# Kernel tuning notes

Hardware: AMD Instinct MI355X
Metric: run time of the kernel (lower is better)

The kernel has to match this reference:

```python
import jax, jax.numpy as jnp
import numpy as np

H, DN, DR, DV, L = 16, 128, 64, 128, 512
EPS = 1e-6

def rotate_half(x):
    x1, x2 = jnp.split(x, 2, axis=-1)
    return jnp.concatenate((-x2, x1), axis=-1)

def setup_inputs() -> dict:
    key = jax.random.key(0)
    ks = jax.random.split(key, 8)
    B, S, HID = 2, 2048, 2048
    inv_freq = 1.0 / (10000.0 ** (jnp.arange(0, DR, 2, dtype=jnp.float32) / DR))
    pos = jnp.arange(B * S, dtype=jnp.float32)
    freqs = pos[:, None] * inv_freq[None, :]
    emb = jnp.concatenate((freqs, freqs), axis=-1)
    return {
        "hidden_states": jax.random.normal(ks[0], (B, S, HID), jnp.float32),
        "cos": jnp.cos(emb),
        "sin": jnp.sin(emb),
        "q_proj_w": jax.random.normal(ks[1], (H * (DN + DR), HID), jnp.float32) * 0.02,
        "kv_a_proj_w": jax.random.normal(ks[2], (L + DR, HID), jnp.float32) * 0.02,
        "kv_a_ln_w": jnp.ones((L,), jnp.float32),
        "W_UK_T": jax.random.normal(ks[3], (H, DN, L), jnp.float32) * 0.02,
        "W_UV": jax.random.normal(ks[4], (H, L, DV), jnp.float32) * 0.02,
        "o_proj_w": jax.random.normal(ks[5], (HID, H * DV), jnp.float32) * 0.02,
    }

def reference(hidden_states, cos, sin, q_proj_w, kv_a_proj_w, kv_a_ln_w, W_UK_T, W_UV, o_proj_w):
    B, S, HID = hidden_states.shape
    T = B * S
    x = hidden_states.reshape(T, HID)
    # q projection -> [T, H, DN+DR]
    q = (x @ q_proj_w.T).reshape(T, H, DN + DR)
    q_pass, q_rot = q[..., :DN], q[..., DN:]
    # compressed kv -> latent + rope key (MQA-style, shared across heads)
    ckv = x @ kv_a_proj_w.T  # [T, L+DR]
    k_pass, k_rot = ckv[..., :L], ckv[..., L:]
    kv_c = k_pass * jax.lax.rsqrt(jnp.mean(k_pass * k_pass, axis=-1, keepdims=True) + EPS) * kv_a_ln_w
    # interleaved RoPE (rope_interleave=True): de-interleave then rotate_half form
    q_rot = q_rot.reshape(T, H, DR // 2, 2).swapaxes(-1, -2).reshape(T, H, DR)
    k_rot = k_rot.reshape(T, DR // 2, 2).swapaxes(-1, -2).reshape(T, DR)
    q_rot = q_rot * cos[:, None, :] + rotate_half(q_rot) * sin[:, None, :]
    k_rot = k_rot * cos + rotate_half(k_rot) * sin
    # absorb W_UK into queries: [T,H,L]
    q_lat = jnp.einsum('thd,hdl->thl', q_pass, W_UK_T)
    q_lat = q_lat.reshape(B, S, H, L)
    q_rot = q_rot.reshape(B, S, H, DR)
    kv_c_b = kv_c.reshape(B, S, L)
    k_rot_b = k_rot.reshape(B, S, DR)
    scale = 1.0 / np.sqrt(DN + DR)
    scores = (jnp.einsum('bshl,btl->bhst', q_lat, kv_c_b)
              + jnp.einsum('bshd,btd->bhst', q_rot, k_rot_b)) * scale
    causal = jnp.tril(jnp.ones((S, S), dtype=bool))
    scores = jnp.where(causal[None, None], scores, jnp.float32(-1e30))
    attn = jax.nn.softmax(scores, axis=-1)
    out_lat = jnp.einsum('bhst,btl->bshl', attn, kv_c_b)   # [B,S,H,L]
    out = jnp.einsum('bshl,hlv->bshv', out_lat, W_UV)       # [B,S,H,DV]
    out = out.reshape(B, S, H * DV) @ o_proj_w.T
    return out
```

## Files before the change

### kernel.cpp

```cpp
#include <hip/hip_runtime.h>
#include <stdint.h>

#define T_TOK 4096
#define HIDD  2048
#define NH    16
#define DNN   128
#define DRR   64
#define DVV   128
#define LAT   512
#define DQK   576
#define SEQ   2048
#define NB    2
#define KSTR  592
#define KCH   2368

typedef __attribute__((__ext_vector_type__(8))) short short8;
typedef __attribute__((__ext_vector_type__(4))) float f32x4;

__device__ __forceinline__ float bf2f(ushort u) {
  union { uint32_t i; float f; } v; v.i = ((uint32_t)u) << 16; return v.f;
}
__device__ __forceinline__ ushort f2bf(float f) {
  union { float f; uint32_t i; } v; v.f = f;
  uint32_t r = v.i + 0x7FFF + ((v.i >> 16) & 1);
  return (ushort)(r >> 16);
}

__device__ __forceinline__ void gld_lds16(const void* g, void* l) {
  __builtin_amdgcn_global_load_lds((const __attribute__((address_space(1))) void*)g,
                                   (__attribute__((address_space(3))) void*)l, 16, 0, 0);
}

__global__ void cast4(const float* __restrict__ in, ushort* __restrict__ out, int n4) {
  int i = blockIdx.x * blockDim.x + threadIdx.x;
  if (i >= n4) return;
  float4 v = ((const float4*)in)[i];
  ushort4 o; o.x = f2bf(v.x); o.y = f2bf(v.y); o.z = f2bf(v.z); o.w = f2bf(v.w);
  ((ushort4*)out)[i] = o;
}

__global__ void cast_pad_kv(const float* __restrict__ in, ushort* __restrict__ out) {
  int i = blockIdx.x * 256 + threadIdx.x;
  int row = (i * 4) >> 11;
  ushort4 o;
  if (row < 576) {
    float4 v = ((const float4*)in)[i];
    o.x = f2bf(v.x); o.y = f2bf(v.y); o.z = f2bf(v.z); o.w = f2bf(v.w);
  } else { o.x = 0; o.y = 0; o.z = 0; o.w = 0; }
  ((ushort4*)out)[i] = o;
}

__global__ void cast_wuk(const float* __restrict__ in, ushort* __restrict__ out) {
  int o = blockIdx.x * 256 + threadIdx.x;
  int d = o & 127, l = (o >> 7) & 511, h = o >> 16;
  out[o] = f2bf(in[((size_t)(h * 128 + d)) * 512 + l]);
}
__global__ void cast_wuv(const float* __restrict__ in, ushort* __restrict__ out) {
  int o = blockIdx.x * 256 + threadIdx.x;
  int l = o & 511, v = (o >> 9) & 127, h = o >> 16;
  out[o] = f2bf(in[((size_t)(h * 512 + l)) * 128 + v]);
}

template<int OUT_BF16>
__global__ __launch_bounds__(256) void gemm_bt(
    const ushort* __restrict__ A, const ushort* __restrict__ B, void* __restrict__ Cv,
    int K, int lda, int ldb, int ldc,
    long long aB, long long bB, long long cB)
{
  __shared__ ushort As[128 * 32];
  __shared__ ushort Bs[128 * 32];
  const int tid = threadIdx.x;
  const int lane = tid & 63, wid = tid >> 6;
  const int m0 = blockIdx.y * 128, n0 = blockIdx.x * 128;
  A += (size_t)blockIdx.z * aB;
  B += (size_t)blockIdx.z * bB;
  const int wm = (wid >> 1) * 64, wn = (wid & 1) * 64;
  const int fr = lane & 15;
  const int kk = (lane >> 4) * 8;
  f32x4 acc[4][4] = {};
  for (int k0 = 0; k0 < K; k0 += 32) {
    __syncthreads();
#pragma unroll
    for (int i = 0; i < 2; ++i) {
      int c = i * 256 + tid;
      gld_lds16(A + (size_t)(m0 + (c >> 2)) * lda + k0 + (c & 3) * 8, (void*)(As + c * 8));
    }
#pragma unroll
    for (int i = 0; i < 2; ++i) {
      int c = i * 256 + tid;
      gld_lds16(B + (size_t)(n0 + (c >> 2)) * ldb + k0 + (c & 3) * 8, (void*)(Bs + c * 8));
    }
    __syncthreads();
    short8 af[4], bf[4];
#pragma unroll
    for (int x = 0; x < 4; ++x) af[x] = *(const short8*)(As + (wm + x * 16 + fr) * 32 + kk);
#pragma unroll
    for (int x = 0; x < 4; ++x) bf[x] = *(const short8*)(Bs + (wn + x * 16 + fr) * 32 + kk);
#pragma unroll
    for (int mi = 0; mi < 4; ++mi)
#pragma unroll
      for (int ni = 0; ni < 4; ++ni)
        acc[mi][ni] = __builtin_amdgcn_mfma_f32_16x16x32_bf16(af[mi], bf[ni], acc[mi][ni], 0, 0, 0);
  }
  const int rb = (lane >> 4) * 4;
#pragma unroll
  for (int mi = 0; mi < 4; ++mi)
#pragma unroll
    for (int ni = 0; ni < 4; ++ni)
#pragma unroll
      for (int r = 0; r < 4; ++r) {
        size_t row = (size_t)(m0 + wm + mi * 16 + rb + r);
        size_t col = (size_t)(n0 + wn + ni * 16 + fr);
        size_t idx = row * (size_t)ldc + col + (size_t)blockIdx.z * cB;
        if (OUT_BF16) ((ushort*)Cv)[idx] = f2bf(acc[mi][ni][r]);
        else          ((float*)Cv)[idx]  = acc[mi][ni][r];
      }
}

__global__ __launch_bounds__(256) void rms_rope_k(
    const float* __restrict__ ckvf, const float* __restrict__ lnw,
    const float* __restrict__ cosb, const float* __restrict__ sinb,
    ushort* __restrict__ k_eff)
{
  const int t = blockIdx.x, tid = threadIdx.x;
  __shared__ float red[4];
  float v0 = ckvf[(size_t)t * 640 + tid];
  float v1 = ckvf[(size_t)t * 640 + 256 + tid];
  float ss = v0 * v0 + v1 * v1;
#pragma unroll
  for (int m = 1; m < 64; m <<= 1) ss += __shfl_xor(ss, m);
  if ((tid & 63) == 0) red[tid >> 6] = ss;
  __syncthreads();
  float rn = rsqrtf((red[0] + red[1] + red[2] + red[3]) * (1.0f / 512.0f) + 1e-6f);
  k_eff[(size_t)t * KSTR + tid]       = f2bf(v0 * rn * lnw[tid]);
  k_eff[(size_t)t * KSTR + 256 + tid] = f2bf(v1 * rn * lnw[256 + tid]);
  if (tid < 64) {
    int j = tid;
    int src  = (j < 32) ? 2 * j : 2 * (j - 32) + 1;
    int psrc = (j < 32) ? src + 1 : src - 1;
    float xv = ckvf[(size_t)t * 640 + 512 + src];
    float pv = ckvf[(size_t)t * 640 + 512 + psrc];
    float c = cosb[t * 64 + j], s = sinb[t * 64 + j];
    k_eff[(size_t)t * KSTR + 512 + j] = f2bf((j < 32) ? xv * c - pv * s : xv * c + pv * s);
  }
}

__global__ __launch_bounds__(256) void transpose_kv(
    const ushort* __restrict__ keff, ushort* __restrict__ kvT)
{
  __shared__ ushort Tl[64][72];
  const int s0 = blockIdx.x * 64, v0 = blockIdx.y * 64, b = blockIdx.z;
  const int tid = threadIdx.x;
#pragma unroll
  for (int i = 0; i < 2; ++i) {
    int c = i * 256 + tid;
    int r = c >> 3, c8 = (c & 7) * 8;
    *(short8*)&Tl[r][c8] = *(const short8*)&keff[((size_t)b * SEQ + s0 + r) * KSTR + v0 + c8];
  }
  __syncthreads();
#pragma unroll
  for (int i = 0; i < 2; ++i) {
    int c = i * 256 + tid;
    int v = c >> 3, s8 = (c & 7) * 8;
    short8 o;
#pragma unroll
    for (int e = 0; e < 8; ++e) o[e] = Tl[s8 + e][v];
    *(short8*)&kvT[((size_t)b * 512 + v0 + v) * SEQ + s0 + s8] = o;
  }
}

__global__ void rope_q(const ushort* __restrict__ qb, const float* __restrict__ cosb,
                       const float* __restrict__ sinb, ushort* __restrict__ q_eff)
{
  const int t = blockIdx.x;
  const int h = blockIdx.y * 4 + threadIdx.y;
  const int j = threadIdx.x;
  size_t base = (size_t)t * 3072 + h * 192 + 128;
  int src  = (j < 32) ? 2 * j : 2 * (j - 32) + 1;
  int psrc = (j < 32) ? src + 1 : src - 1;
  float xv = bf2f(qb[base + src]), pv = bf2f(qb[base + psrc]);
  float c = cosb[t * 64 + j], s = sinb[t * 64 + j];
  q_eff[((size_t)h * T_TOK + t) * DQK + 512 + j] = f2bf((j < 32) ? xv * c - pv * s : xv * c + pv * s);
}

__global__ __launch_bounds__(512, 2) void attn3(
    const ushort* __restrict__ q_eff, const ushort* __restrict__ keff,
    const ushort* __restrict__ kvT, ushort* __restrict__ out_lat)
{
  const int pair = blockIdx.x;
  const int h = blockIdx.y, b = blockIdx.z;
  const int tid = threadIdx.x, lane = tid & 63, w = tid >> 6;
  __shared__ ushort Ks[2][32 * KSTR];
  __shared__ ushort Vt[2][512 * 32];
  __shared__ ushort Pl[8][16 * 40];

  const int fr = lane & 15, g = lane >> 4;

  auto stageK = [&](int kt, int buf) {
    const ushort* ksrc = keff + ((size_t)b * SEQ + (size_t)kt * 32) * KSTR;
    ushort* kd = &Ks[buf][0];
#pragma unroll
    for (int i = 0; i < 5; ++i) {
      int c0 = w * 320 + i * 64;
      if (c0 < KCH) {
        int c = c0 + lane;
        gld_lds16(ksrc + (size_t)c * 8, (void*)(kd + (size_t)c * 8));
      }
    }
  };
  auto stageV = [&](int kt, int buf) {
    const ushort* vsrc = kvT + (size_t)b * 512 * SEQ + (size_t)kt * 32;
    ushort* vd = &Vt[buf][0];
#pragma unroll
    for (int i = 0; i < 4; ++i) {
      int c = w * 256 + i * 64 + lane;
      gld_lds16(vsrc + (size_t)(c >> 2) * SEQ + (c & 3) * 8, (void*)(vd + (size_t)c * 8));
    }
  };

  for (int half = 0; half < 2; ++half) {
    const int qb = half ? pair : (15 - pair);
    const int q0 = qb * 128 + w * 16;

    const ushort* qrow = q_eff + ((size_t)h * T_TOK + (size_t)b * SEQ + q0 + fr) * DQK + g * 8;
    short8 qf[18];
#pragma unroll
    for (int ks = 0; ks < 18; ++ks) qf[ks] = *(const short8*)(qrow + ks * 32);

    f32x4 acc[32] = {};
    float m_s[4] = {-1e30f, -1e30f, -1e30f, -1e30f};
    float l_s[4] = {0.f, 0.f, 0.f, 0.f};

    const int nt = 4 * qb + 4;

    stageK(0, 0);
    stageV(0, 0);

    for (int kt = 0; kt < nt; ++kt) {
      const int cur = kt & 1;
      if (kt + 1 < nt) {
        stageK(kt + 1, cur ^ 1);
        stageV(kt + 1, cur ^ 1);
        if (w == 7) asm volatile("s_waitcnt vmcnt(6)" ::: "memory");
        else        asm volatile("s_waitcnt vmcnt(9)" ::: "memory");
      } else {
        asm volatile("s_waitcnt vmcnt(0)" ::: "memory");
      }
      __builtin_amdgcn_sched_barrier(0);
      __builtin_amdgcn_s_barrier();
      __builtin_amdgcn_sched_barrier(0);

      if (kt * 32 <= q0 + 15) {
        const ushort* Kc = &Ks[cur][0];
        const ushort* Vc = &Vt[cur][0];
        f32x4 s0 = {}, s1 = {};
#pragma unroll
        for (int ks = 0; ks < 18; ++ks) {
          short8 b0 = *(const short8*)(Kc + (0 * 16 + fr) * KSTR + ks * 32 + g * 8);
          short8 b1 = *(const short8*)(Kc + (1 * 16 + fr) * KSTR + ks * 32 + g * 8);
          s0 = __builtin_amdgcn_mfma_f32_16x16x32_bf16(qf[ks], b0, s0, 0, 0, 0);
          s1 = __builtin_amdgcn_mfma_f32_16x16x32_bf16(qf[ks], b1, s1, 0, 0, 0);
        }
        const float SC = 0.07216878364870322f;
        const bool diag = (kt * 32 + 31 > q0);
        float sv0[4], sv1[4];
#pragma unroll
        for (int r = 0; r < 4; ++r) {
          int qg = q0 + 4 * g + r;
          float a0 = s0[r] * SC, a1 = s1[r] * SC;
          if (diag) {
            if (kt * 32 + fr > qg)      a0 = -1e30f;
            if (kt * 32 + 16 + fr > qg) a1 = -1e30f;
          }
          sv0[r] = a0; sv1[r] = a1;
        }
        float mx[4];
#pragma unroll
        for (int r = 0; r < 4; ++r) {
          float m2 = fmaxf(sv0[r], sv1[r]);
          m2 = fmaxf(m2, __shfl_xor(m2, 1));
          m2 = fmaxf(m2, __shfl_xor(m2, 2));
          m2 = fmaxf(m2, __shfl_xor(m2, 4));
          m2 = fmaxf(m2, __shfl_xor(m2, 8));
          mx[r] = m2;
        }
        float need = mx[0] - m_s[0];
#pragma unroll
        for (int r = 1; r < 4; ++r) need = fmaxf(need, mx[r] - m_s[r]);
        if (__any(need > 8.0f)) {
          float rsc[4];
#pragma unroll
          for (int r = 0; r < 4; ++r) {
            float mn = fmaxf(m_s[r], mx[r]);
            rsc[r] = __expf(m_s[r] - mn);
            m_s[r] = mn;
            l_s[r] *= rsc[r];
          }
#pragma unroll
          for (int n2 = 0; n2 < 32; ++n2)
#pragma unroll
            for (int r = 0; r < 4; ++r) acc[n2][r] *= rsc[r];
        }
        float p0[4], p1[4];
#pragma unroll
        for (int r = 0; r < 4; ++r) {
          p0[r] = __expf(sv0[r] - m_s[r]);
          p1[r] = __expf(sv1[r] - m_s[r]);
          float ps = p0[r] + p1[r];
          ps += __shfl_xor(ps, 1);
          ps += __shfl_xor(ps, 2);
          ps += __shfl_xor(ps, 4);
          ps += __shfl_xor(ps, 8);
          l_s[r] += ps;
          Pl[w][(4 * g + r) * 40 + fr]      = f2bf(p0[r]);
          Pl[w][(4 * g + r) * 40 + 16 + fr] = f2bf(p1[r]);
        }
        short8 pa = *(const short8*)(Pl[w] + fr * 40 + g * 8);
#pragma unroll
        for (int n2 = 0; n2 < 32; ++n2) {
          short8 bv = *(const short8*)(Vc + (n2 * 16 + fr) * 32 + g * 8);
          acc[n2] = __builtin_amdgcn_mfma_f32_16x16x32_bf16(pa, bv, acc[n2], 0, 0, 0);
        }
      }
      __builtin_amdgcn_sched_barrier(0);
      __builtin_amdgcn_s_barrier();
      __builtin_amdgcn_sched_barrier(0);
    }

    const size_t obase = ((size_t)h * T_TOK + (size_t)b * SEQ + q0) * LAT;
    float inv[4];
#pragma unroll
    for (int r = 0; r < 4; ++r) inv[r] = 1.0f / l_s[r];
#pragma unroll
    for (int n2 = 0; n2 < 32; ++n2)
#pragma unroll
      for (int r = 0; r < 4; ++r)
        out_lat[obase + (size_t)(4 * g + r) * LAT + n2 * 16 + fr] = f2bf(acc[n2][r] * inv[r]);
  }
}

extern "C" void kernel_launch(void* const* d_in, const int* in_sizes, int n_in,
                              void* d_out, int out_size, void* d_ws, size_t ws_size,
                              hipStream_t stream) {
  const float* hs   = (const float*)d_in[0];
  const float* cosb = (const float*)d_in[1];
  const float* sinb = (const float*)d_in[2];
  const float* qw   = (const float*)d_in[3];
  const float* kvw  = (const float*)d_in[4];
  const float* lnw  = (const float*)d_in[5];
  const float* wuk  = (const float*)d_in[6];
  const float* wuv  = (const float*)d_in[7];
  const float* wo   = (const float*)d_in[8];
  float* out = (float*)d_out;
  char* ws = (char*)d_ws;

  const size_t o_xb   = 0;
  const size_t o_qb   = 16777216;
  const size_t o_wq   = 41943040;
  const size_t o_wkv  = 54525952;
  const size_t o_ckv  = 57147392;
  const size_t o_ol   = 0;
  const size_t o_wukt = 67633152;
  const size_t o_wuvt = 69730304;
  const size_t o_wo   = 71827456;
  const size_t o_keff = 80216064;
  const size_t o_qeff = 85065728;
  const size_t o_oh   = 160563200;
  const size_t o_kvt  = 177340416;

  ushort* xb    = (ushort*)(ws + o_xb);
  ushort* qbuf  = (ushort*)(ws + o_qb);
  ushort* wq_b  = (ushort*)(ws + o_wq);
  ushort* wkv_b = (ushort*)(ws + o_wkv);
  float*  ckvf  = (float*)(ws + o_ckv);
  ushort* olat  = (ushort*)(ws + o_ol);
  ushort* wukt  = (ushort*)(ws + o_wukt);
  ushort* wuvt  = (ushort*)(ws + o_wuvt);
  ushort* wo_b  = (ushort*)(ws + o_wo);
  ushort* keff  = (ushort*)(ws + o_keff);
  ushort* qeff  = (ushort*)(ws + o_qeff);
  ushort* ohead = (ushort*)(ws + o_oh);
  ushort* kvt   = (ushort*)(ws + o_kvt);

  cast4<<<8192, 256, 0, stream>>>(hs, xb, 8388608 / 4);
  cast4<<<6144, 256, 0, stream>>>(qw, wq_b, 6291456 / 4);
  cast_pad_kv<<<1280, 256, 0, stream>>>(kvw, wkv_b);
  cast4<<<4096, 256, 0, stream>>>(wo, wo_b, 4194304 / 4);
  cast_wuk<<<4096, 256, 0, stream>>>(wuk, wukt);
  cast_wuv<<<4096, 256, 0, stream>>>(wuv, wuvt);

  gemm_bt<1><<<dim3(24, 32, 1), 256, 0, stream>>>(xb, wq_b, qbuf, 2048, 2048, 2048, 3072, 0, 0, 0);
  gemm_bt<0><<<dim3(5, 32, 1), 256, 0, stream>>>(xb, wkv_b, ckvf, 2048, 2048, 2048, 640, 0, 0, 0);
  rms_rope_k<<<4096, 256, 0, stream>>>(ckvf, lnw, cosb, sinb, keff);
  transpose_kv<<<dim3(32, 8, 2), 256, 0, stream>>>(keff, kvt);
  rope_q<<<dim3(4096, 4, 1), dim3(64, 4, 1), 0, stream>>>(qbuf, cosb, sinb, qeff);
  gemm_bt<1><<<dim3(4, 32, 16), 256, 0, stream>>>(qbuf, wukt, qeff, 128, 3072, 128, 576,
                                                  192LL, 65536LL, 2359296LL);
  attn3<<<dim3(8, 16, 2), 512, 0, stream>>>(qeff, keff, kvt, olat);
  gemm_bt<1><<<dim3(1, 32, 16), 256, 0, stream>>>(olat, wuvt, ohead, 512, 512, 512, 2048,
                                                  2097152LL, 65536LL, 128LL);
  gemm_bt<0><<<dim3(16, 32, 1), 256, 0, stream>>>(ohead, wo_b, out, 2048, 2048, 2048, 2048, 0, 0, 0);
}
```

Baseline: 684.8 us.

## Double-buffer GEMM LDS staging and merge q and kv_a projections

The bf16 GEMM now double-buffers its LDS tiles and prefetches the next K slice while MFMAs run on the current one, using explicit vmcnt waits and barriers. The q projection and kv_a projection are merged into one GEMM with a 3712-wide output. The compressed-KV part now comes out as bf16 rather than fp32, and the downstream RMSNorm/RoPE and q-absorb kernels read from the merged buffer. This removes one launch and one pass over the activations and hides load latency, but the KV latent is now rounded to bf16 before normalization and the GEMM uses twice the LDS.

```diff
diff --git a/kernel.cpp b/kernel.cpp
--- a/kernel.cpp
+++ b/kernel.cpp
@@ -13,6 +13,7 @@
 #define NB    2
 #define KSTR  592
 #define KCH   2368
+#define QCKV  3712
 
 typedef __attribute__((__ext_vector_type__(8))) short short8;
 typedef __attribute__((__ext_vector_type__(4))) float f32x4;
@@ -67,8 +68,8 @@
     int K, int lda, int ldb, int ldc,
     long long aB, long long bB, long long cB)
 {
-  __shared__ ushort As[128 * 32];
-  __shared__ ushort Bs[128 * 32];
+  __shared__ ushort As[2][128 * 32];
+  __shared__ ushort Bs[2][128 * 32];
   const int tid = threadIdx.x;
   const int lane = tid & 63, wid = tid >> 6;
   const int m0 = blockIdx.y * 128, n0 = blockIdx.x * 128;
@@ -77,31 +78,51 @@
   const int wm = (wid >> 1) * 64, wn = (wid & 1) * 64;
   const int fr = lane & 15;
   const int kk = (lane >> 4) * 8;
-  f32x4 acc[4][4] = {};
-  for (int k0 = 0; k0 < K; k0 += 32) {
-    __syncthreads();
+
+  auto stage = [&](int k0, int buf) {
 #pragma unroll
     for (int i = 0; i < 2; ++i) {
       int c = i * 256 + tid;
-      gld_lds16(A + (size_t)(m0 + (c >> 2)) * lda + k0 + (c & 3) * 8, (void*)(As + c * 8));
+      gld_lds16(A + (size_t)(m0 + (c >> 2)) * lda + k0 + (c & 3) * 8, (void*)(&As[buf][0] + c * 8));
     }
 #pragma unroll
     for (int i = 0; i < 2; ++i) {
       int c = i * 256 + tid;
-      gld_lds16(B + (size_t)(n0 + (c >> 2)) * ldb + k0 + (c & 3) * 8, (void*)(Bs + c * 8));
-    }
-    __syncthreads();
+      gld_lds16(B + (size_t)(n0 + (c >> 2)) * ldb + k0 + (c & 3) * 8, (void*)(&Bs[buf][0] + c * 8));
+    }
+  };
+
+  f32x4 acc[4][4] = {};
+  const int nt = K >> 5;
+  stage(0, 0);
+  for (int t = 0; t < nt; ++t) {
+    const int cur = t & 1;
+    if (t + 1 < nt) {
+      stage((t + 1) << 5, cur ^ 1);
+      asm volatile("s_waitcnt vmcnt(4)" ::: "memory");
+    } else {
+      asm volatile("s_waitcnt vmcnt(0)" ::: "memory");
+    }
+    __builtin_amdgcn_sched_barrier(0);
+    __builtin_amdgcn_s_barrier();
+    __builtin_amdgcn_sched_barrier(0);
+
     short8 af[4], bf[4];
 #pragma unroll
-    for (int x = 0; x < 4; ++x) af[x] = *(const short8*)(As + (wm + x * 16 + fr) * 32 + kk);
-#pragma unroll
-    for (int x = 0; x < 4; ++x) bf[x] = *(const short8*)(Bs + (wn + x * 16 + fr) * 32 + kk);
+    for (int x = 0; x < 4; ++x) af[x] = *(const short8*)(&As[cur][0] + (wm + x * 16 + fr) * 32 + kk);
+#pragma unroll
+    for (int x = 0; x < 4; ++x) bf[x] = *(const short8*)(&Bs[cur][0] + (wn + x * 16 + fr) * 32 + kk);
 #pragma unroll
     for (int mi = 0; mi < 4; ++mi)
 #pragma unroll
       for (int ni = 0; ni < 4; ++ni)
         acc[mi][ni] = __builtin_amdgcn_mfma_f32_16x16x32_bf16(af[mi], bf[ni], acc[mi][ni], 0, 0, 0);
+
+    __builtin_amdgcn_sched_barrier(0);
+    __builtin_amdgcn_s_barrier();
+    __builtin_amdgcn_sched_barrier(0);
   }
+
   const int rb = (lane >> 4) * 4;
 #pragma unroll
   for (int mi = 0; mi < 4; ++mi)
@@ -118,14 +139,15 @@
 }
 
 __global__ __launch_bounds__(256) void rms_rope_k(
-    const float* __restrict__ ckvf, const float* __restrict__ lnw,
+    const ushort* __restrict__ qckv, const float* __restrict__ lnw,
     const float* __restrict__ cosb, const float* __restrict__ sinb,
     ushort* __restrict__ k_eff)
 {
   const int t = blockIdx.x, tid = threadIdx.x;
   __shared__ float red[4];
-  float v0 = ckvf[(size_t)t * 640 + tid];
-  float v1 = ckvf[(size_t)t * 640 + 256 + tid];
+  const size_t base = (size_t)t * QCKV + 3072;
+  float v0 = bf2f(qckv[base + tid]);
+  float v1 = bf2f(qckv[base + 256 + tid]);
   float ss = v0 * v0 + v1 * v1;
 #pragma unroll
   for (int m = 1; m < 64; m <<= 1) ss += __shfl_xor(ss, m);
@@ -138,8 +160,8 @@
     int j = tid;
     int src  = (j < 32) ? 2 * j : 2 * (j - 32) + 1;
     int psrc = (j < 32) ? src + 1 : src - 1;
-    float xv = ckvf[(size_t)t * 640 + 512 + src];
-    float pv = ckvf[(size_t)t * 640 + 512 + psrc];
+    float xv = bf2f(qckv[base + 512 + src]);
+    float pv = bf2f(qckv[base + 512 + psrc]);
     float c = cosb[t * 64 + j], s = sinb[t * 64 + j];
     k_eff[(size_t)t * KSTR + 512 + j] = f2bf((j < 32) ? xv * c - pv * s : xv * c + pv * s);
   }
@@ -175,7 +197,7 @@
   const int t = blockIdx.x;
   const int h = blockIdx.y * 4 + threadIdx.y;
   const int j = threadIdx.x;
-  size_t base = (size_t)t * 3072 + h * 192 + 128;
+  size_t base = (size_t)t * QCKV + h * 192 + 128;
   int src  = (j < 32) ? 2 * j : 2 * (j - 32) + 1;
   int psrc = (j < 32) ? src + 1 : src - 1;
   float xv = bf2f(qb[base + src]), pv = bf2f(qb[base + psrc]);
@@ -356,23 +378,21 @@
 
   const size_t o_xb   = 0;
   const size_t o_qb   = 16777216;
-  const size_t o_wq   = 41943040;
-  const size_t o_wkv  = 54525952;
-  const size_t o_ckv  = 57147392;
+  const size_t o_wq   = 47185920;
+  const size_t o_wkv  = 59768832;
   const size_t o_ol   = 0;
-  const size_t o_wukt = 67633152;
-  const size_t o_wuvt = 69730304;
-  const size_t o_wo   = 71827456;
-  const size_t o_keff = 80216064;
-  const size_t o_qeff = 85065728;
-  const size_t o_oh   = 160563200;
-  const size_t o_kvt  = 177340416;
+  const size_t o_wukt = 67108864;
+  const size_t o_wuvt = 69206016;
+  const size_t o_wo   = 71303168;
+  const size_t o_keff = 79691776;
+  const size_t o_qeff = 84541440;
+  const size_t o_oh   = 160038912;
+  const size_t o_kvt  = 176816128;
 
   ushort* xb    = (ushort*)(ws + o_xb);
   ushort* qbuf  = (ushort*)(ws + o_qb);
   ushort* wq_b  = (ushort*)(ws + o_wq);
   ushort* wkv_b = (ushort*)(ws + o_wkv);
-  float*  ckvf  = (float*)(ws + o_ckv);
   ushort* olat  = (ushort*)(ws + o_ol);
   ushort* wukt  = (ushort*)(ws + o_wukt);
   ushort* wuvt  = (ushort*)(ws + o_wuvt);
@@ -389,12 +409,11 @@
   cast_wuk<<<4096, 256, 0, stream>>>(wuk, wukt);
   cast_wuv<<<4096, 256, 0, stream>>>(wuv, wuvt);
 
-  gemm_bt<1><<<dim3(24, 32, 1), 256, 0, stream>>>(xb, wq_b, qbuf, 2048, 2048, 2048, 3072, 0, 0, 0);
-  gemm_bt<0><<<dim3(5, 32, 1), 256, 0, stream>>>(xb, wkv_b, ckvf, 2048, 2048, 2048, 640, 0, 0, 0);
-  rms_rope_k<<<4096, 256, 0, stream>>>(ckvf, lnw, cosb, sinb, keff);
+  gemm_bt<1><<<dim3(29, 32, 1), 256, 0, stream>>>(xb, wq_b, qbuf, 2048, 2048, 2048, QCKV, 0, 0, 0);
+  rms_rope_k<<<4096, 256, 0, stream>>>(qbuf, lnw, cosb, sinb, keff);
   transpose_kv<<<dim3(32, 8, 2), 256, 0, stream>>>(keff, kvt);
   rope_q<<<dim3(4096, 4, 1), dim3(64, 4, 1), 0, stream>>>(qbuf, cosb, sinb, qeff);
-  gemm_bt<1><<<dim3(4, 32, 16), 256, 0, stream>>>(qbuf, wukt, qeff, 128, 3072, 128, 576,
+  gemm_bt<1><<<dim3(4, 32, 16), 256, 0, stream>>>(qbuf, wukt, qeff, 128, QCKV, 128, 576,
                                                   192LL, 65536LL, 2359296LL);
   attn3<<<dim3(8, 16, 2), 512, 0, stream>>>(qeff, keff, kvt, olat);
   gemm_bt<1><<<dim3(1, 32, 16), 256, 0, stream>>>(olat, wuvt, ohead, 512, 512, 512, 2048,
```

After: 662.3 us. -3.3%, faster.
